# Optimization experiments

Hardware: AMD Instinct MI355X
Metric: run time of the kernel (lower is better)

The kernel has to match this reference:

```python
import jax, jax.numpy as jnp
import numpy as np

N, P, C = 100000, 64, 128
DIST_TH = 0.1


def setup_inputs() -> dict:
    key = jax.random.key(0)
    ks = jax.random.split(key, 12)
    xyz = jax.random.uniform(ks[0], (N, 3), jnp.float32) * 10.0  # room coords in [0,10)^3
    feature = jax.random.normal(ks[1], (N, C), jnp.float32)
    center = jax.random.uniform(ks[2], (P, 3), jnp.float32) * 10.0
    normal = jax.random.normal(ks[3], (P, 3), jnp.float32)
    normal = normal / jnp.linalg.norm(normal, axis=1, keepdims=True)
    pmin = center - 1.5  # axis-aligned extent used on axes 0,1
    pmax = center + 1.5
    inp = {
        'feature': feature, 'xyz': xyz,
        'plane_center': center, 'plane_normal': normal,
        'plane_min': pmin, 'plane_max': pmax,
        'W1': jax.random.normal(ks[4], (C, 2 * C), jnp.float32) * (1.0 / np.sqrt(C)),
        's1': jnp.ones((2 * C,), jnp.float32), 'b1': jnp.zeros((2 * C,), jnp.float32),
        'W2': jax.random.normal(ks[5], (2 * C, C), jnp.float32) * (1.0 / np.sqrt(2 * C)),
        's2': jnp.ones((C,), jnp.float32), 'b2': jnp.zeros((C,), jnp.float32),
        'W3': jax.random.normal(ks[6], (C, 1), jnp.float32) * (1.0 / np.sqrt(C)),
        'b3': jnp.zeros((1,), jnp.float32),
        'Wa': jax.random.normal(ks[7], (C, C), jnp.float32) * (1.0 / np.sqrt(C)),
        'Wm': jax.random.normal(ks[8], (C, C), jnp.float32) * (1.0 / np.sqrt(C)),
        'bm': jnp.zeros((C,), jnp.float32),
    }
    return inp


def reference(feature, xyz, plane_center, plane_normal, plane_min, plane_max,
              W1, s1, b1, W2, s2, b2, W3, b3, Wa, Wm, bm):
    # pointwise MLP (shared across planes): fc1 (conv+BN+ReLU), fc2 (conv+BN+ReLU)
    h = jax.nn.relu((feature @ W1) * s1 + b1)          # [N, 2C]
    h2 = jax.nn.relu((h @ W2) * s2 + b2)               # [N, C] == plane_feature
    logit = (h2 @ W3 + b3)[:, 0]                        # [N] fc3 logits (plane_result)

    # per-plane point membership masks (dense [N, P])
    proj = xyz @ plane_normal.T                         # [N, P]
    offs = jnp.sum(plane_center * plane_normal, axis=1) # [P]
    dist_mask = jnp.abs(proj - offs[None, :]) < DIST_TH
    rng = ((xyz[:, None, 0] >= plane_min[None, :, 0]) & (xyz[:, None, 0] < plane_max[None, :, 0]) &
           (xyz[:, None, 1] >= plane_min[None, :, 1]) & (xyz[:, None, 1] < plane_max[None, :, 1]))
    mask = dist_mask & rng                              # [N, P]

    on_sel = jax.nn.sigmoid(logit) > 0.5                # [N]
    on_mask = (mask & on_sel[:, None]).astype(feature.dtype)
    off_mask = (mask & ~on_sel[:, None]).astype(feature.dtype)

    # attention pooling: masked softmax over points, per plane, per channel
    a = h2 @ Wa                                         # [N, C] att activations
    e = jnp.exp(a - jnp.max(a, axis=0, keepdims=True))  # stable exp, [N, C]
    eh = e * h2

    def att_pool(m):                                    # m: [N, P] float
        num = jnp.einsum('np,nc->pc', m, eh)
        den = jnp.einsum('np,nc->pc', m, e)
        agg = num / (den + 1e-9)                        # masked-softmax weighted sum
        return jax.nn.relu(agg @ Wm + bm)               # att_pooling.mlp (conv+ReLU)

    ori = jnp.concatenate([plane_center, plane_normal, plane_min, plane_max], axis=1)  # [P, 12]
    on_feat = jnp.concatenate([att_pool(on_mask), ori], axis=1)    # [P, C+12]
    off_feat = jnp.concatenate([att_pool(off_mask), ori], axis=1)  # [P, C+12]
    return logit, on_feat, off_feat
```

## Files before the change

### kernel.cpp

```cpp
#include <hip/hip_runtime.h>

#define NPTS 100000
#define P 64
#define C 128
#define CHUNKS 16
#define CHUNK_PTS 6250
#define CHUNK_PAD 6400

typedef __bf16 bf16_t;
typedef __bf16 bf16x8 __attribute__((ext_vector_type(8)));
typedef float floatx4 __attribute__((ext_vector_type(4)));


__global__ __launch_bounds__(256) void prep_kernel(
    const float* __restrict__ W1, const float* __restrict__ s1,
    const float* __restrict__ W2, const float* __restrict__ s2,
    const float* __restrict__ Wa,
    bf16_t* __restrict__ W1t, bf16_t* __restrict__ W2t, bf16_t* __restrict__ Wat)
{
  int i0 = blockIdx.x * blockDim.x + threadIdx.x;
  int stride = gridDim.x * blockDim.x;
  for (int i = i0; i < 256 * 128; i += stride) {
    int n = i >> 7, k = i & 127;
    W1t[i] = (bf16_t)(W1[k * 256 + n] * s1[n]);
  }
  for (int i = i0; i < 128 * 256; i += stride) {
    int n = i >> 8, k = i & 255;
    W2t[i] = (bf16_t)(W2[k * 128 + n] * s2[n]);
  }
  for (int i = i0; i < 128 * 128; i += stride) {
    int n = i >> 7, k = i & 127;
    Wat[i] = (bf16_t)(Wa[k * 128 + n]);
  }
}

__global__ __launch_bounds__(256) void main_kernel(
    const float* __restrict__ feature,
    const float* __restrict__ b1, const float* __restrict__ b2,
    const float* __restrict__ W3, const float* __restrict__ b3,
    const bf16_t* __restrict__ W1t, const bf16_t* __restrict__ W2t,
    const bf16_t* __restrict__ Wat,
    bf16_t* __restrict__ rec, float* __restrict__ out_logit)
{
  __shared__ __align__(16) char smem[17408 + 33792 + 512];
  bf16_t* A1  = (bf16_t*)smem;
  bf16_t* Hs  = (bf16_t*)(smem + 17408);
  bf16_t* aB  = (bf16_t*)(smem + 17408);
  float*  w3S = (float*)(smem + 17408 + 33792);

  const int tid  = threadIdx.x;
  const int wave = tid >> 6, lane = tid & 63;
  const int quad = lane >> 4, l16 = lane & 15;
  const int m0 = blockIdx.x * 64;

  if (tid < 128) w3S[tid] = W3[tid];

  for (int i = tid; i < 64 * 32; i += 256) {
    int r = i >> 5, c4 = i & 31;
    float4 v = make_float4(0.f, 0.f, 0.f, 0.f);
    if (m0 + r < NPTS) v = *(const float4*)(feature + (size_t)(m0 + r) * C + c4 * 4);
    bf16_t* dst = A1 + r * 136 + c4 * 4;
    dst[0] = (bf16_t)v.x; dst[1] = (bf16_t)v.y; dst[2] = (bf16_t)v.z; dst[3] = (bf16_t)v.w;
  }
  __syncthreads();

  const floatx4 zero4 = {0.f, 0.f, 0.f, 0.f};

  {
    floatx4 acc[4][4];
#pragma unroll
    for (int mt = 0; mt < 4; ++mt)
#pragma unroll
      for (int nt = 0; nt < 4; ++nt) acc[mt][nt] = zero4;
#pragma unroll
    for (int kt = 0; kt < 4; ++kt) {
      bf16x8 af[4], bf[4];
#pragma unroll
      for (int mt = 0; mt < 4; ++mt)
        af[mt] = *(const bf16x8*)(A1 + (mt * 16 + l16) * 136 + kt * 32 + quad * 8);
#pragma unroll
      for (int nt = 0; nt < 4; ++nt)
        bf[nt] = *(const bf16x8*)(W1t + (wave * 64 + nt * 16 + l16) * 128 + kt * 32 + quad * 8);
#pragma unroll
      for (int mt = 0; mt < 4; ++mt)
#pragma unroll
        for (int nt = 0; nt < 4; ++nt)
          acc[mt][nt] = __builtin_amdgcn_mfma_f32_16x16x32_bf16(af[mt], bf[nt], acc[mt][nt], 0, 0, 0);
    }
#pragma unroll
    for (int nt = 0; nt < 4; ++nt) {
      int col = wave * 64 + nt * 16 + l16;
      float bias = b1[col];
#pragma unroll
      for (int mt = 0; mt < 4; ++mt)
#pragma unroll
        for (int r = 0; r < 4; ++r) {
          float hv = fmaxf(acc[mt][nt][r] + bias, 0.f);
          Hs[(mt * 16 + quad * 4 + r) * 264 + col] = (bf16_t)hv;
        }
    }
  }
  __syncthreads();

  {
    floatx4 acc[4][2];
#pragma unroll
    for (int mt = 0; mt < 4; ++mt) { acc[mt][0] = zero4; acc[mt][1] = zero4; }
#pragma unroll
    for (int kt = 0; kt < 8; ++kt) {
      bf16x8 af[4], bf[2];
#pragma unroll
      for (int mt = 0; mt < 4; ++mt)
        af[mt] = *(const bf16x8*)(Hs + (mt * 16 + l16) * 264 + kt * 32 + quad * 8);
#pragma unroll
      for (int nt = 0; nt < 2; ++nt)
        bf[nt] = *(const bf16x8*)(W2t + (wave * 32 + nt * 16 + l16) * 256 + kt * 32 + quad * 8);
#pragma unroll
      for (int mt = 0; mt < 4; ++mt)
#pragma unroll
        for (int nt = 0; nt < 2; ++nt)
          acc[mt][nt] = __builtin_amdgcn_mfma_f32_16x16x32_bf16(af[mt], bf[nt], acc[mt][nt], 0, 0, 0);
    }
#pragma unroll
    for (int nt = 0; nt < 2; ++nt) {
      int col = wave * 32 + nt * 16 + l16;
      float bias = b2[col];
#pragma unroll
      for (int mt = 0; mt < 4; ++mt)
#pragma unroll
        for (int r = 0; r < 4; ++r) {
          float hv = fmaxf(acc[mt][nt][r] + bias, 0.f);
          A1[(mt * 16 + quad * 4 + r) * 136 + col] = (bf16_t)hv;
        }
    }
  }
  __syncthreads();

  {
    floatx4 acc[4][2];
#pragma unroll
    for (int mt = 0; mt < 4; ++mt) { acc[mt][0] = zero4; acc[mt][1] = zero4; }
#pragma unroll
    for (int kt = 0; kt < 4; ++kt) {
      bf16x8 af[4], bf[2];
#pragma unroll
      for (int mt = 0; mt < 4; ++mt)
        af[mt] = *(const bf16x8*)(A1 + (mt * 16 + l16) * 136 + kt * 32 + quad * 8);
#pragma unroll
      for (int nt = 0; nt < 2; ++nt)
        bf[nt] = *(const bf16x8*)(Wat + (wave * 32 + nt * 16 + l16) * 128 + kt * 32 + quad * 8);
#pragma unroll
      for (int mt = 0; mt < 4; ++mt)
#pragma unroll
        for (int nt = 0; nt < 2; ++nt)
          acc[mt][nt] = __builtin_amdgcn_mfma_f32_16x16x32_bf16(af[mt], bf[nt], acc[mt][nt], 0, 0, 0);
    }
#pragma unroll
    for (int nt = 0; nt < 2; ++nt) {
      int col = wave * 32 + nt * 16 + l16;
#pragma unroll
      for (int mt = 0; mt < 4; ++mt)
#pragma unroll
        for (int r = 0; r < 4; ++r)
          aB[(mt * 16 + quad * 4 + r) * 136 + col] = (bf16_t)acc[mt][nt][r];
    }
  }
  __syncthreads();

  {
    const int m = tid >> 2, g = tid & 3, c0g = g * 32;
    const int mg = m0 + m;
    float lsum = 0.f;
#pragma unroll 8
    for (int c = 0; c < 32; ++c)
      lsum += (float)A1[m * 136 + c0g + c] * w3S[c0g + c];
    lsum += __shfl_xor(lsum, 1);
    lsum += __shfl_xor(lsum, 2);
    if (mg < NPTS && g == 0) out_logit[mg] = lsum + b3[0];
  }

  for (int i = tid; i < 64 * 64; i += 256) {
    int pt = i >> 6, slot = i & 63;
    if (m0 + pt < NPTS) {
      const bf16_t* src = (slot < 32) ? (aB + pt * 136 + slot * 4)
                                      : (A1 + pt * 136 + (slot - 32) * 4);
      uint2 v = *(const uint2*)src;
      *(uint2*)(rec + (size_t)(m0 + pt) * 256 + slot * 4) = v;
    }
  }
}

__global__ __launch_bounds__(256) void pool_kernel(
    const float* __restrict__ xyz, const float* __restrict__ out_logit,
    const bf16_t* __restrict__ rec,
    const float* __restrict__ ctr, const float* __restrict__ nrm,
    const float* __restrict__ pmn, const float* __restrict__ pmx,
    float* __restrict__ partial)
{
  const int plane = blockIdx.x >> 4;
  const int chunk = blockIdx.x & 15;
  const int tid = threadIdx.x, lane = tid & 63;

  __shared__ float accS[4][128];
  for (int i = tid; i < 512; i += 256) ((float*)accS)[i] = 0.f;

  const float nx = nrm[plane * 3], ny = nrm[plane * 3 + 1], nz = nrm[plane * 3 + 2];
  const float offs = ctr[plane * 3] * nx + ctr[plane * 3 + 1] * ny + ctr[plane * 3 + 2] * nz;
  const float mnx = pmn[plane * 3], mny = pmn[plane * 3 + 1];
  const float mxx = pmx[plane * 3], mxy = pmx[plane * 3 + 1];
  __syncthreads();

  const int base = chunk * CHUNK_PTS;
  float nOn0 = 0, nOn1 = 0, dOn0 = 0, dOn1 = 0;
  float nOf0 = 0, nOf1 = 0, dOf0 = 0, dOf1 = 0;

  for (int i = tid; i < CHUNK_PAD; i += 256) {
    int pt = base + i;
    bool hit = false;
    if (i < CHUNK_PTS) {
      float x = xyz[pt * 3], y = xyz[pt * 3 + 1], z = xyz[pt * 3 + 2];
      float proj = x * nx + y * ny + z * nz;
      hit = (fabsf(proj - offs) < 0.1f) &&
            (x >= mnx) && (x < mxx) && (y >= mny) && (y < mxy);
    }
    unsigned long long m = __ballot(hit);
    while (m) {
      int l = __builtin_ctzll(m);
      m &= m - 1;
      int hpt = __shfl(pt, l);
      float lg = out_logit[hpt];
      const unsigned* r32 = (const unsigned*)(rec + (size_t)hpt * 256);
      unsigned ap = r32[lane];
      unsigned hp = r32[64 + lane];
      float a0 = __uint_as_float(ap << 16);
      float a1 = __uint_as_float(ap & 0xffff0000u);
      float h0 = __uint_as_float(hp << 16);
      float h1 = __uint_as_float(hp & 0xffff0000u);
      float e0 = __expf(a0), e1 = __expf(a1);
      if (lg > 0.f) { nOn0 += e0 * h0; nOn1 += e1 * h1; dOn0 += e0; dOn1 += e1; }
      else          { nOf0 += e0 * h0; nOf1 += e1 * h1; dOf0 += e0; dOf1 += e1; }
    }
  }

  atomicAdd(&accS[0][lane * 2],     nOn0);
  atomicAdd(&accS[0][lane * 2 + 1], nOn1);
  atomicAdd(&accS[1][lane * 2],     dOn0);
  atomicAdd(&accS[1][lane * 2 + 1], dOn1);
  atomicAdd(&accS[2][lane * 2],     nOf0);
  atomicAdd(&accS[2][lane * 2 + 1], nOf1);
  atomicAdd(&accS[3][lane * 2],     dOf0);
  atomicAdd(&accS[3][lane * 2 + 1], dOf1);
  __syncthreads();

  float* dst = partial + (size_t)blockIdx.x * 512;
  for (int i = tid; i < 512; i += 256) dst[i] = ((float*)accS)[i];
}

__global__ __launch_bounds__(128) void finalize_kernel(
    const float* __restrict__ partial,
    const float* __restrict__ Wm, const float* __restrict__ bm,
    const float* __restrict__ ctr, const float* __restrict__ nrm,
    const float* __restrict__ pmn, const float* __restrict__ pmx,
    float* __restrict__ out)
{
  int sel = blockIdx.x >> 6, p = blockIdx.x & 63;
  int j = threadIdx.x;
  float num = 0.f, den = 0.f;
  const float* bp = partial + (size_t)p * 16 * 512 + sel * 2 * 128;
#pragma unroll
  for (int k = 0; k < 16; ++k) {
    num += bp[k * 512 + j];
    den += bp[k * 512 + 128 + j];
  }
  __shared__ float aggS[128];
  aggS[j] = num / (den + 1e-9f);
  __syncthreads();
  float s = bm[j];
#pragma unroll 4
  for (int c = 0; c < C; ++c) s += aggS[c] * Wm[c * C + j];
  s = fmaxf(s, 0.f);
  float* dst = out + NPTS + sel * (P * 140) + p * 140;
  dst[j] = s;
  if (j < 12) {
    float v;
    if (j < 3)      v = ctr[p * 3 + j];
    else if (j < 6) v = nrm[p * 3 + j - 3];
    else if (j < 9) v = pmn[p * 3 + j - 6];
    else            v = pmx[p * 3 + j - 9];
    dst[C + j] = v;
  }
}

extern "C" void kernel_launch(void* const* d_in, const int* in_sizes, int n_in,
                              void* d_out, int out_size, void* d_ws, size_t ws_size,
                              hipStream_t stream)
{
  const float* feature = (const float*)d_in[0];
  const float* xyz     = (const float*)d_in[1];
  const float* ctr     = (const float*)d_in[2];
  const float* nrm     = (const float*)d_in[3];
  const float* pmn     = (const float*)d_in[4];
  const float* pmx     = (const float*)d_in[5];
  const float* W1      = (const float*)d_in[6];
  const float* s1      = (const float*)d_in[7];
  const float* b1      = (const float*)d_in[8];
  const float* W2      = (const float*)d_in[9];
  const float* s2      = (const float*)d_in[10];
  const float* b2      = (const float*)d_in[11];
  const float* W3      = (const float*)d_in[12];
  const float* b3      = (const float*)d_in[13];
  const float* Wa      = (const float*)d_in[14];
  const float* Wm      = (const float*)d_in[15];
  const float* bm      = (const float*)d_in[16];
  float* out = (float*)d_out;

  char* ws = (char*)d_ws;
  bf16_t* W1t = (bf16_t*)(ws);
  bf16_t* W2t = (bf16_t*)(ws + 65536);
  bf16_t* Wat = (bf16_t*)(ws + 131072);
  bf16_t* rec = (bf16_t*)(ws + 163840);
  float* partial = (float*)(ws + 163840 + (size_t)NPTS * 512);

  prep_kernel<<<64, 256, 0, stream>>>(W1, s1, W2, s2, Wa, W1t, W2t, Wat);
  main_kernel<<<(NPTS + 63) / 64, 256, 0, stream>>>(
      feature, b1, b2, W3, b3, W1t, W2t, Wat, rec, out);
  pool_kernel<<<64 * CHUNKS, 256, 0, stream>>>(
      xyz, out, rec, ctr, nrm, pmn, pmx, partial);
  finalize_kernel<<<128, 128, 0, stream>>>(partial, Wm, bm, ctr, nrm, pmn, pmx, out);
}
```

Baseline: 197.5 us.

## Fuse plane membership and attention pooling into MLP kernel with global atomics

Moves the per-plane membership test and the exp-weighted accumulation into the main MLP kernel, reading activations straight from shared memory instead of writing and regathering a per-point bf16 record buffer. Each wave handles 16 points with one plane per lane and scatters the results into a global per-plane accumulator using float atomics; the accumulator is zeroed in the prep kernel. This removes the large intermediate write, the separate pool kernel, and the partial-sum reduction in finalize. The trade-off is many contended global atomics on a small set of addresses and an order-dependent floating-point summation.

```diff
diff --git a/kernel.cpp b/kernel.cpp
--- a/kernel.cpp
+++ b/kernel.cpp
@@ -3,9 +3,6 @@
 #define NPTS 100000
 #define P 64
 #define C 128
-#define CHUNKS 16
-#define CHUNK_PTS 6250
-#define CHUNK_PAD 6400
 
 typedef __bf16 bf16_t;
 typedef __bf16 bf16x8 __attribute__((ext_vector_type(8)));
@@ -16,7 +13,8 @@
     const float* __restrict__ W1, const float* __restrict__ s1,
     const float* __restrict__ W2, const float* __restrict__ s2,
     const float* __restrict__ Wa,
-    bf16_t* __restrict__ W1t, bf16_t* __restrict__ W2t, bf16_t* __restrict__ Wat)
+    bf16_t* __restrict__ W1t, bf16_t* __restrict__ W2t, bf16_t* __restrict__ Wat,
+    float* __restrict__ acc)
 {
   int i0 = blockIdx.x * blockDim.x + threadIdx.x;
   int stride = gridDim.x * blockDim.x;
@@ -32,21 +30,26 @@
     int n = i >> 7, k = i & 127;
     Wat[i] = (bf16_t)(Wa[k * 128 + n]);
   }
+  for (int i = i0; i < P * 512; i += stride) acc[i] = 0.f;
 }
 
 __global__ __launch_bounds__(256) void main_kernel(
-    const float* __restrict__ feature,
+    const float* __restrict__ feature, const float* __restrict__ xyz,
     const float* __restrict__ b1, const float* __restrict__ b2,
     const float* __restrict__ W3, const float* __restrict__ b3,
+    const float* __restrict__ ctr, const float* __restrict__ nrm,
+    const float* __restrict__ pmn, const float* __restrict__ pmx,
     const bf16_t* __restrict__ W1t, const bf16_t* __restrict__ W2t,
     const bf16_t* __restrict__ Wat,
-    bf16_t* __restrict__ rec, float* __restrict__ out_logit)
-{
-  __shared__ __align__(16) char smem[17408 + 33792 + 512];
-  bf16_t* A1  = (bf16_t*)smem;
-  bf16_t* Hs  = (bf16_t*)(smem + 17408);
-  bf16_t* aB  = (bf16_t*)(smem + 17408);
-  float*  w3S = (float*)(smem + 17408 + 33792);
+    float* __restrict__ acc, float* __restrict__ out_logit)
+{
+  __shared__ __align__(16) char smem[52736];
+  bf16_t* A1   = (bf16_t*)smem;
+  bf16_t* Hs   = (bf16_t*)(smem + 17408);
+  bf16_t* aB   = (bf16_t*)(smem + 17408);
+  float*  w3S  = (float*)(smem + 51200);
+  float*  xyzS = (float*)(smem + 51712);
+  float*  lgS  = (float*)(smem + 52480);
 
   const int tid  = threadIdx.x;
   const int wave = tid >> 6, lane = tid & 63;
@@ -54,6 +57,10 @@
   const int m0 = blockIdx.x * 64;
 
   if (tid < 128) w3S[tid] = W3[tid];
+  if (tid < 192) {
+    int gi = m0 * 3 + tid;
+    xyzS[tid] = (gi < NPTS * 3) ? xyz[gi] : 0.f;
+  }
 
   for (int i = tid; i < 64 * 32; i += 256) {
     int r = i >> 5, c4 = i & 31;
@@ -67,25 +74,25 @@
   const floatx4 zero4 = {0.f, 0.f, 0.f, 0.f};
 
   {
-    floatx4 acc[4][4];
+    floatx4 acc1[4][4];
 #pragma unroll
     for (int mt = 0; mt < 4; ++mt)
 #pragma unroll
-      for (int nt = 0; nt < 4; ++nt) acc[mt][nt] = zero4;
+      for (int nt = 0; nt < 4; ++nt) acc1[mt][nt] = zero4;
 #pragma unroll
     for (int kt = 0; kt < 4; ++kt) {
-      bf16x8 af[4], bf[4];
+      bf16x8 af[4], bfr[4];
 #pragma unroll
       for (int mt = 0; mt < 4; ++mt)
         af[mt] = *(const bf16x8*)(A1 + (mt * 16 + l16) * 136 + kt * 32 + quad * 8);
 #pragma unroll
       for (int nt = 0; nt < 4; ++nt)
-        bf[nt] = *(const bf16x8*)(W1t + (wave * 64 + nt * 16 + l16) * 128 + kt * 32 + quad * 8);
+        bfr[nt] = *(const bf16x8*)(W1t + (wave * 64 + nt * 16 + l16) * 128 + kt * 32 + quad * 8);
 #pragma unroll
       for (int mt = 0; mt < 4; ++mt)
 #pragma unroll
         for (int nt = 0; nt < 4; ++nt)
-          acc[mt][nt] = __builtin_amdgcn_mfma_f32_16x16x32_bf16(af[mt], bf[nt], acc[mt][nt], 0, 0, 0);
+          acc1[mt][nt] = __builtin_amdgcn_mfma_f32_16x16x32_bf16(af[mt], bfr[nt], acc1[mt][nt], 0, 0, 0);
     }
 #pragma unroll
     for (int nt = 0; nt < 4; ++nt) {
@@ -95,7 +102,7 @@
       for (int mt = 0; mt < 4; ++mt)
 #pragma unroll
         for (int r = 0; r < 4; ++r) {
-          float hv = fmaxf(acc[mt][nt][r] + bias, 0.f);
+          float hv = fmaxf(acc1[mt][nt][r] + bias, 0.f);
           Hs[(mt * 16 + quad * 4 + r) * 264 + col] = (bf16_t)hv;
         }
     }
@@ -103,23 +110,23 @@
   __syncthreads();
 
   {
-    floatx4 acc[4][2];
-#pragma unroll
-    for (int mt = 0; mt < 4; ++mt) { acc[mt][0] = zero4; acc[mt][1] = zero4; }
+    floatx4 acc2[4][2];
+#pragma unroll
+    for (int mt = 0; mt < 4; ++mt) { acc2[mt][0] = zero4; acc2[mt][1] = zero4; }
 #pragma unroll
     for (int kt = 0; kt < 8; ++kt) {
-      bf16x8 af[4], bf[2];
+      bf16x8 af[4], bfr[2];
 #pragma unroll
       for (int mt = 0; mt < 4; ++mt)
         af[mt] = *(const bf16x8*)(Hs + (mt * 16 + l16) * 264 + kt * 32 + quad * 8);
 #pragma unroll
       for (int nt = 0; nt < 2; ++nt)
-        bf[nt] = *(const bf16x8*)(W2t + (wave * 32 + nt * 16 + l16) * 256 + kt * 32 + quad * 8);
+        bfr[nt] = *(const bf16x8*)(W2t + (wave * 32 + nt * 16 + l16) * 256 + kt * 32 + quad * 8);
 #pragma unroll
       for (int mt = 0; mt < 4; ++mt)
 #pragma unroll
         for (int nt = 0; nt < 2; ++nt)
-          acc[mt][nt] = __builtin_amdgcn_mfma_f32_16x16x32_bf16(af[mt], bf[nt], acc[mt][nt], 0, 0, 0);
+          acc2[mt][nt] = __builtin_amdgcn_mfma_f32_16x16x32_bf16(af[mt], bfr[nt], acc2[mt][nt], 0, 0, 0);
     }
 #pragma unroll
     for (int nt = 0; nt < 2; ++nt) {
@@ -129,7 +136,7 @@
       for (int mt = 0; mt < 4; ++mt)
 #pragma unroll
         for (int r = 0; r < 4; ++r) {
-          float hv = fmaxf(acc[mt][nt][r] + bias, 0.f);
+          float hv = fmaxf(acc2[mt][nt][r] + bias, 0.f);
           A1[(mt * 16 + quad * 4 + r) * 136 + col] = (bf16_t)hv;
         }
     }
@@ -137,23 +144,23 @@
   __syncthreads();
 
   {
-    floatx4 acc[4][2];
-#pragma unroll
-    for (int mt = 0; mt < 4; ++mt) { acc[mt][0] = zero4; acc[mt][1] = zero4; }
+    floatx4 acca[4][2];
+#pragma unroll
+    for (int mt = 0; mt < 4; ++mt) { acca[mt][0] = zero4; acca[mt][1] = zero4; }
 #pragma unroll
     for (int kt = 0; kt < 4; ++kt) {
-      bf16x8 af[4], bf[2];
+      bf16x8 af[4], bfr[2];
 #pragma unroll
       for (int mt = 0; mt < 4; ++mt)
         af[mt] = *(const bf16x8*)(A1 + (mt * 16 + l16) * 136 + kt * 32 + quad * 8);
 #pragma unroll
       for (int nt = 0; nt < 2; ++nt)
-        bf[nt] = *(const bf16x8*)(Wat + (wave * 32 + nt * 16 + l16) * 128 + kt * 32 + quad * 8);
+        bfr[nt] = *(const bf16x8*)(Wat + (wave * 32 + nt * 16 + l16) * 128 + kt * 32 + quad * 8);
 #pragma unroll
       for (int mt = 0; mt < 4; ++mt)
 #pragma unroll
         for (int nt = 0; nt < 2; ++nt)
-          acc[mt][nt] = __builtin_amdgcn_mfma_f32_16x16x32_bf16(af[mt], bf[nt], acc[mt][nt], 0, 0, 0);
+          acca[mt][nt] = __builtin_amdgcn_mfma_f32_16x16x32_bf16(af[mt], bfr[nt], acca[mt][nt], 0, 0, 0);
     }
 #pragma unroll
     for (int nt = 0; nt < 2; ++nt) {
@@ -162,7 +169,7 @@
       for (int mt = 0; mt < 4; ++mt)
 #pragma unroll
         for (int r = 0; r < 4; ++r)
-          aB[(mt * 16 + quad * 4 + r) * 136 + col] = (bf16_t)acc[mt][nt][r];
+          aB[(mt * 16 + quad * 4 + r) * 136 + col] = (bf16_t)acca[mt][nt][r];
     }
   }
   __syncthreads();
@@ -176,88 +183,55 @@
       lsum += (float)A1[m * 136 + c0g + c] * w3S[c0g + c];
     lsum += __shfl_xor(lsum, 1);
     lsum += __shfl_xor(lsum, 2);
-    if (mg < NPTS && g == 0) out_logit[mg] = lsum + b3[0];
-  }
-
-  for (int i = tid; i < 64 * 64; i += 256) {
-    int pt = i >> 6, slot = i & 63;
-    if (m0 + pt < NPTS) {
-      const bf16_t* src = (slot < 32) ? (aB + pt * 136 + slot * 4)
-                                      : (A1 + pt * 136 + (slot - 32) * 4);
-      uint2 v = *(const uint2*)src;
-      *(uint2*)(rec + (size_t)(m0 + pt) * 256 + slot * 4) = v;
-    }
-  }
-}
-
-__global__ __launch_bounds__(256) void pool_kernel(
-    const float* __restrict__ xyz, const float* __restrict__ out_logit,
-    const bf16_t* __restrict__ rec,
-    const float* __restrict__ ctr, const float* __restrict__ nrm,
-    const float* __restrict__ pmn, const float* __restrict__ pmx,
-    float* __restrict__ partial)
-{
-  const int plane = blockIdx.x >> 4;
-  const int chunk = blockIdx.x & 15;
-  const int tid = threadIdx.x, lane = tid & 63;
-
-  __shared__ float accS[4][128];
-  for (int i = tid; i < 512; i += 256) ((float*)accS)[i] = 0.f;
-
-  const float nx = nrm[plane * 3], ny = nrm[plane * 3 + 1], nz = nrm[plane * 3 + 2];
-  const float offs = ctr[plane * 3] * nx + ctr[plane * 3 + 1] * ny + ctr[plane * 3 + 2] * nz;
-  const float mnx = pmn[plane * 3], mny = pmn[plane * 3 + 1];
-  const float mxx = pmx[plane * 3], mxy = pmx[plane * 3 + 1];
-  __syncthreads();
-
-  const int base = chunk * CHUNK_PTS;
-  float nOn0 = 0, nOn1 = 0, dOn0 = 0, dOn1 = 0;
-  float nOf0 = 0, nOf1 = 0, dOf0 = 0, dOf1 = 0;
-
-  for (int i = tid; i < CHUNK_PAD; i += 256) {
-    int pt = base + i;
-    bool hit = false;
-    if (i < CHUNK_PTS) {
-      float x = xyz[pt * 3], y = xyz[pt * 3 + 1], z = xyz[pt * 3 + 2];
-      float proj = x * nx + y * ny + z * nz;
-      hit = (fabsf(proj - offs) < 0.1f) &&
-            (x >= mnx) && (x < mxx) && (y >= mny) && (y < mxy);
-    }
-    unsigned long long m = __ballot(hit);
-    while (m) {
-      int l = __builtin_ctzll(m);
-      m &= m - 1;
-      int hpt = __shfl(pt, l);
-      float lg = out_logit[hpt];
-      const unsigned* r32 = (const unsigned*)(rec + (size_t)hpt * 256);
-      unsigned ap = r32[lane];
-      unsigned hp = r32[64 + lane];
-      float a0 = __uint_as_float(ap << 16);
-      float a1 = __uint_as_float(ap & 0xffff0000u);
-      float h0 = __uint_as_float(hp << 16);
-      float h1 = __uint_as_float(hp & 0xffff0000u);
-      float e0 = __expf(a0), e1 = __expf(a1);
-      if (lg > 0.f) { nOn0 += e0 * h0; nOn1 += e1 * h1; dOn0 += e0; dOn1 += e1; }
-      else          { nOf0 += e0 * h0; nOf1 += e1 * h1; dOf0 += e0; dOf1 += e1; }
-    }
-  }
-
-  atomicAdd(&accS[0][lane * 2],     nOn0);
-  atomicAdd(&accS[0][lane * 2 + 1], nOn1);
-  atomicAdd(&accS[1][lane * 2],     dOn0);
-  atomicAdd(&accS[1][lane * 2 + 1], dOn1);
-  atomicAdd(&accS[2][lane * 2],     nOf0);
-  atomicAdd(&accS[2][lane * 2 + 1], nOf1);
-  atomicAdd(&accS[3][lane * 2],     dOf0);
-  atomicAdd(&accS[3][lane * 2 + 1], dOf1);
-  __syncthreads();
-
-  float* dst = partial + (size_t)blockIdx.x * 512;
-  for (int i = tid; i < 512; i += 256) dst[i] = ((float*)accS)[i];
+    if (g == 0) {
+      float lg = lsum + b3[0];
+      lgS[m] = lg;
+      if (mg < NPTS) out_logit[mg] = lg;
+    }
+  }
+  __syncthreads();
+
+  {
+    const float nx = nrm[lane * 3], ny = nrm[lane * 3 + 1], nz = nrm[lane * 3 + 2];
+    const float offsP = ctr[lane * 3] * nx + ctr[lane * 3 + 1] * ny + ctr[lane * 3 + 2] * nz;
+    const float mnx = pmn[lane * 3], mny = pmn[lane * 3 + 1];
+    const float mxx = pmx[lane * 3], mxy = pmx[lane * 3 + 1];
+
+    for (int s = 0; s < 16; ++s) {
+      const int pt = wave * 16 + s;
+      const bool valid = (m0 + pt) < NPTS;
+      const float x = xyzS[pt * 3], y = xyzS[pt * 3 + 1], z = xyzS[pt * 3 + 2];
+      const float proj = x * nx + y * ny + z * nz;
+      const bool hit = valid && (fabsf(proj - offsP) < 0.1f) &&
+                       (x >= mnx) && (x < mxx) && (y >= mny) && (y < mxy);
+      unsigned long long mball = __ballot(hit);
+      if (!mball) continue;
+
+      const int sel = (lgS[pt] > 0.f) ? 0 : 1;
+      const unsigned ap = ((const unsigned*)(aB + pt * 136))[lane];
+      const unsigned hp = ((const unsigned*)(A1 + pt * 136))[lane];
+      const float a0 = __uint_as_float(ap << 16);
+      const float a1 = __uint_as_float(ap & 0xffff0000u);
+      const float h0 = __uint_as_float(hp << 16);
+      const float h1 = __uint_as_float(hp & 0xffff0000u);
+      const float e0 = __expf(a0), e1 = __expf(a1);
+      const float eh0 = e0 * h0, eh1 = e1 * h1;
+
+      while (mball) {
+        const int pl = __builtin_ctzll(mball);
+        mball &= mball - 1;
+        float* ab = acc + (size_t)pl * 512 + sel * 256;
+        atomicAdd(ab + 2 * lane,           eh0);
+        atomicAdd(ab + 2 * lane + 1,       eh1);
+        atomicAdd(ab + 128 + 2 * lane,     e0);
+        atomicAdd(ab + 128 + 2 * lane + 1, e1);
+      }
+    }
+  }
 }
 
 __global__ __launch_bounds__(128) void finalize_kernel(
-    const float* __restrict__ partial,
+    const float* __restrict__ acc,
     const float* __restrict__ Wm, const float* __restrict__ bm,
     const float* __restrict__ ctr, const float* __restrict__ nrm,
     const float* __restrict__ pmn, const float* __restrict__ pmx,
@@ -265,13 +239,8 @@
 {
   int sel = blockIdx.x >> 6, p = blockIdx.x & 63;
   int j = threadIdx.x;
-  float num = 0.f, den = 0.f;
-  const float* bp = partial + (size_t)p * 16 * 512 + sel * 2 * 128;
-#pragma unroll
-  for (int k = 0; k < 16; ++k) {
-    num += bp[k * 512 + j];
-    den += bp[k * 512 + 128 + j];
-  }
+  const float* ab = acc + (size_t)p * 512 + sel * 256;
+  float num = ab[j], den = ab[128 + j];
   __shared__ float aggS[128];
   aggS[j] = num / (den + 1e-9f);
   __syncthreads();
@@ -318,13 +287,10 @@
   bf16_t* W1t = (bf16_t*)(ws);
   bf16_t* W2t = (bf16_t*)(ws + 65536);
   bf16_t* Wat = (bf16_t*)(ws + 131072);
-  bf16_t* rec = (bf16_t*)(ws + 163840);
-  float* partial = (float*)(ws + 163840 + (size_t)NPTS * 512);
-
-  prep_kernel<<<64, 256, 0, stream>>>(W1, s1, W2, s2, Wa, W1t, W2t, Wat);
+  float*  acc = (float*)(ws + 163840);
+
+  prep_kernel<<<64, 256, 0, stream>>>(W1, s1, W2, s2, Wa, W1t, W2t, Wat, acc);
   main_kernel<<<(NPTS + 63) / 64, 256, 0, stream>>>(
-      feature, b1, b2, W3, b3, W1t, W2t, Wat, rec, out);
-  pool_kernel<<<64 * CHUNKS, 256, 0, stream>>>(
-      xyz, out, rec, ctr, nrm, pmn, pmx, partial);
-  finalize_kernel<<<128, 128, 0, stream>>>(partial, Wm, bm, ctr, nrm, pmn, pmx, out);
-}
+      feature, xyz, b1, b2, W3, b3, ctr, nrm, pmn, pmx, W1t, W2t, Wat, acc, out);
+  finalize_kernel<<<128, 128, 0, stream>>>(acc, Wm, bm, ctr, nrm, pmn, pmx, out);
+}
```

Result: slower. 220.7 us (+11.7%).
